# Optimization experiments

Measured on AMD Instinct MI355X. Metric: run time of the kernel, lower is better.

## Reference

```python
import jax, jax.numpy as jnp
import numpy as np

EPS = 1e-6
H = 16
CHUNK = 128

def _fmap(x):
    # elu(x) + 1 positive feature map
    return jax.nn.elu(x) + 1.0

def _causal_lin_attn(Qf, Kf, V, eps):
    # Math-identical chunkwise form of the cumsum causal linear attention.
    B, Hh, N, D = Qf.shape
    Dv = V.shape[-1]
    nc = N // CHUNK
    qs = jnp.moveaxis(Qf.reshape(B, Hh, nc, CHUNK, D), 2, 0)
    ks = jnp.moveaxis(Kf.reshape(B, Hh, nc, CHUNK, D), 2, 0)
    vs = jnp.moveaxis(V.reshape(B, Hh, nc, CHUNK, Dv), 2, 0)
    mask = jnp.tril(jnp.ones((CHUNK, CHUNK), dtype=bool))  # inclusive causal within chunk
    S0 = jnp.zeros((B, Hh, D, Dv), Qf.dtype)
    z0 = jnp.zeros((B, Hh, D), Qf.dtype)

    def step(carry, xs):
        S, z = carry
        q, k, v = xs  # (B,H,C,D), (B,H,C,D), (B,H,C,Dv)
        A = jnp.einsum('bhqd,bhkd->bhqk', q, k)
        A = jnp.where(mask, A, 0.0)
        num = jnp.einsum('bhqd,bhdv->bhqv', q, S) + jnp.einsum('bhqk,bhkv->bhqv', A, v)
        den = jnp.einsum('bhqd,bhd->bhq', q, z) + A.sum(-1)
        out = num / (den[..., None] + eps)
        S = S + jnp.einsum('bhkd,bhkv->bhdv', k, v)
        z = z + k.sum(2)
        return (S, z), out

    _, out = jax.lax.scan(step, (S0, z0), (qs, ks, vs))
    return jnp.moveaxis(out, 0, 2).reshape(B, Hh, N, Dv)

def _mhla(Q, K, V, Wq, Wk, Wv, Wo, causal):
    B, N, E = Q.shape
    D = E // H
    q = (Q @ Wq.T).reshape(B, N, H, D).transpose(0, 2, 1, 3)  # (B,H,N,D)
    k = (K @ Wk.T).reshape(B, N, H, D).transpose(0, 2, 1, 3)
    v = (V @ Wv.T).reshape(B, N, H, D).transpose(0, 2, 1, 3)
    Qf, Kf = _fmap(q), _fmap(k)
    if causal:
        out = _causal_lin_attn(Qf, Kf, v, EPS)
    else:
        KV = jnp.einsum('bhnd,bhnv->bhdv', Kf, v)
        ksum = Kf.sum(2)
        num = jnp.einsum('bhnd,bhdv->bhnv', Qf, KV)
        den = jnp.einsum('bhnd,bhd->bhn', Qf, ksum)[..., None]
        out = num / (den + EPS)
    out = out.transpose(0, 2, 1, 3).reshape(B, N, E)
    return out @ Wo.T

def setup_inputs():
    key = jax.random.key(0)
    ks = jax.random.split(key, 7)
    B, N, E = 2, 2048, 1024

    def xavier(k, shape):
        lim = (6.0 / (shape[0] + shape[1])) ** 0.5
        return jax.random.uniform(k, shape, jnp.float32, -lim, lim)

    return {
        'Q': jax.random.normal(ks[0], (B, N, E), jnp.float32),
        'K': jax.random.normal(ks[1], (B, N, E), jnp.float32),
        'V': jax.random.normal(ks[2], (B, N, E), jnp.float32),
        'Wq': xavier(ks[3], (E, E)),
        'Wk': xavier(ks[4], (E, E)),
        'Wv': xavier(ks[5], (E, E)),
        'Wo': xavier(ks[6], (E, E)),
        'causal': 1,
    }

def reference(Q, K, V, Wq, Wk, Wv, Wo, causal):
    return _mhla(Q, K, V, Wq, Wk, Wv, Wo, causal)
```

## Files before the change

kernel.cpp:

```cpp
#include <hip/hip_runtime.h>
#include <hip/hip_bf16.h>
#include <stdint.h>

#define B_   2
#define N_   2048
#define E_   1024
#define H_   16
#define D_   64
#define CH_  128
#define NC_  16
#define BH_  32
#define M_   4096
#define K_   1024
#define EPS_F 1e-6f

typedef __attribute__((ext_vector_type(8))) __bf16 bf16x8;
typedef __attribute__((ext_vector_type(4))) float  f32x4;

static __device__ __forceinline__ f32x4 mfma16(bf16x8 a, bf16x8 b, f32x4 c) {
  return __builtin_amdgcn_mfma_f32_16x16x32_bf16(a, b, c, 0, 0, 0);
}

static __device__ __forceinline__ unsigned short f2bf(float f) {
  union { float fv; unsigned int u; } x; x.fv = f;
  unsigned int r = x.u + 0x7FFFu + ((x.u >> 16) & 1u);
  return (unsigned short)(r >> 16);
}
static __device__ __forceinline__ float fmap(float x) {
  return x > 0.f ? (x + 1.f) : __expf(x);
}
static __device__ __forceinline__ void gload16(const void* g, void* l) {
  __builtin_amdgcn_global_load_lds(
      (const __attribute__((address_space(1))) void*)g,
      (__attribute__((address_space(3))) void*)l, 16, 0, 0);
}

__global__ __launch_bounds__(256)
void conv_kernel(const float* __restrict__ Q, const float* __restrict__ Kx,
                 const float* __restrict__ V, const float* __restrict__ Wq,
                 const float* __restrict__ Wk, const float* __restrict__ Wv,
                 const float* __restrict__ Wo,
                 unsigned short* __restrict__ Xb, unsigned short* __restrict__ Wb) {
  int gid = blockIdx.x * 256 + threadIdx.x;
  int idx = gid * 4;
  const float* src; unsigned short* dst; int off;
  if (idx < (3 << 22)) {
    int which = idx >> 22;
    off = idx & ((1 << 22) - 1);
    src = (which == 0) ? Q : (which == 1) ? Kx : V;
    dst = Xb + ((size_t)which << 22);
  } else {
    int j = idx - (3 << 22);
    int which = j >> 20;
    off = j & ((1 << 20) - 1);
    src = (which == 0) ? Wq : (which == 1) ? Wk : (which == 2) ? Wv : Wo;
    dst = Wb + ((size_t)which << 20);
  }
  float4 v = *(const float4*)(src + off);
  ushort4 o;
  o.x = f2bf(v.x); o.y = f2bf(v.y); o.z = f2bf(v.z); o.w = f2bf(v.w);
  *(ushort4*)(dst + off) = o;
}

template<int MODE>
__global__ __launch_bounds__(256)
void gemm_kernel(const unsigned short* __restrict__ Aall,
                 const unsigned short* __restrict__ Wall,
                 unsigned short* __restrict__ qf,
                 unsigned short* __restrict__ kf,
                 unsigned short* __restrict__ kt,
                 unsigned short* __restrict__ vt,
                 float* __restrict__ outf) {
  constexpr int BM = (MODE == 0) ? 128 : 64;
  constexpr int WM = BM / 32;
  constexpr int NWG = (MODE == 0) ? 768 : 512;
  __shared__ __align__(16) unsigned short As[BM * 32];
  __shared__ __align__(16) unsigned short Bs[128 * 32];

  const int wg = (blockIdx.x & 7) * (NWG >> 3) + (blockIdx.x >> 3);
  const int nb = wg & 7;
  const int mb = (MODE == 0) ? ((wg >> 3) & 31) : (wg >> 3);
  const int z  = (MODE == 0) ? (wg >> 8) : 3;

  const unsigned short* Ag = Aall + ((MODE == 0) ? ((size_t)z << 22) : 0);
  const unsigned short* Bg = Wall + ((size_t)z << 20);
  const int tid = threadIdx.x;
  const int w = tid >> 6, l = tid & 63;
  const int wm = w >> 1, wn = w & 1;
  const int fl = l & 15, fh = l >> 4;
  const int lrow = l >> 2;
  const int swz = (l & 3) ^ ((l >> 3) & 3);

  const unsigned short* gA = Ag + (size_t)(mb * BM + w * (BM / 4) + lrow) * K_ + swz * 8;
  const unsigned short* gB = Bg + (size_t)(nb * 128 + w * 32 + lrow) * K_ + swz * 8;
  unsigned short* lA = As + w * (BM / 4) * 32;
  unsigned short* lB = Bs + w * 1024;

  const int rs = (fh ^ ((fl >> 1) & 3)) * 8;

  f32x4 acc[WM][4] = {};

  for (int k0 = 0; k0 < K_; k0 += 32) {
    __syncthreads();
    gload16(gA + k0, lA);
    if (MODE == 0) gload16(gA + k0 + 16 * K_, lA + 512);
    gload16(gB + k0, lB);
    gload16(gB + k0 + 16 * K_, lB + 512);
    __syncthreads();
    bf16x8 av[WM], bv[4];
#pragma unroll
    for (int i = 0; i < WM; i++)
      av[i] = *(const bf16x8*)(As + (wm * (BM / 2) + i * 16 + fl) * 32 + rs);
#pragma unroll
    for (int j = 0; j < 4; j++)
      bv[j] = *(const bf16x8*)(Bs + (wn * 64 + j * 16 + fl) * 32 + rs);
#pragma unroll
    for (int i = 0; i < WM; i++)
#pragma unroll
      for (int j = 0; j < 4; j++)
        acc[i][j] = mfma16(av[i], bv[j], acc[i][j]);
  }

#pragma unroll
  for (int i = 0; i < WM; i++)
#pragma unroll
    for (int j = 0; j < 4; j++)
#pragma unroll
      for (int r = 0; r < 4; r++) {
        int m = mb * BM + wm * (BM / 2) + i * 16 + fh * 4 + r;
        int e = nb * 128 + wn * 64 + j * 16 + fl;
        float v = acc[i][j][r];
        if (MODE == 1) {
          outf[(size_t)m * E_ + e] = v;
        } else {
          int b = m >> 11, n = m & (N_ - 1), h = e >> 6, d = e & 63;
          int bh = b * H_ + h;
          if (z == 0) {
            qf[((size_t)bh * N_ + n) * D_ + d] = f2bf(fmap(v));
          } else if (z == 1) {
            unsigned short s = f2bf(fmap(v));
            kf[((size_t)bh * N_ + n) * D_ + d] = s;
            kt[((size_t)bh * D_ + d) * N_ + n] = s;
          } else {
            vt[((size_t)bh * D_ + d) * N_ + n] = f2bf(v);
          }
        }
      }
}

__global__ __launch_bounds__(64)
void chunkkv_kernel(const unsigned short* __restrict__ kt,
                    const unsigned short* __restrict__ vt,
                    float* __restrict__ Sc, float* __restrict__ zc) {
  const int bh = blockIdx.x, c = blockIdx.y;
  const int l = threadIdx.x;
  const int fl = l & 15, fh = l >> 4;
  const int n0 = c * CH_;
  const unsigned short* ktb = kt + (size_t)bh * D_ * N_;
  const unsigned short* vtb = vt + (size_t)bh * D_ * N_;
  f32x4 acc[4][4] = {};
#pragma unroll
  for (int ks = 0; ks < 4; ks++) {
    bf16x8 av[4], bv[4];
#pragma unroll
    for (int i = 0; i < 4; i++)
      av[i] = *(const bf16x8*)(vtb + (size_t)(i * 16 + fl) * N_ + n0 + ks * 32 + fh * 8);
#pragma unroll
    for (int j = 0; j < 4; j++)
      bv[j] = *(const bf16x8*)(ktb + (size_t)(j * 16 + fl) * N_ + n0 + ks * 32 + fh * 8);
#pragma unroll
    for (int i = 0; i < 4; i++)
#pragma unroll
      for (int j = 0; j < 4; j++)
        acc[i][j] = mfma16(av[i], bv[j], acc[i][j]);
  }
  float* Scb = Sc + ((size_t)(bh * NC_ + c) << 12);
#pragma unroll
  for (int i = 0; i < 4; i++)
#pragma unroll
    for (int j = 0; j < 4; j++)
#pragma unroll
      for (int r = 0; r < 4; r++)
        Scb[(i * 16 + fh * 4 + r) * 64 + j * 16 + fl] = acc[i][j][r];
  float s = 0.f;
  const unsigned short* kr = ktb + (size_t)l * N_ + n0;
#pragma unroll
  for (int t = 0; t < 16; t++) {
    bf16x8 v8 = *(const bf16x8*)(kr + t * 8);
#pragma unroll
    for (int e = 0; e < 8; e++) s += (float)v8[e];
  }
  zc[(bh * NC_ + c) * 64 + l] = s;
}

__global__ __launch_bounds__(256)
void prefix_kernel(const float* __restrict__ Sc, const float* __restrict__ zc,
                   unsigned short* __restrict__ St, float* __restrict__ zx) {
  int gid = blockIdx.x * 256 + threadIdx.x;
  if (blockIdx.x < 512) {
    int bh = gid >> 12;
    int idx = gid & 4095;
    float s = 0.f;
    for (int c = 0; c < NC_; c++) {
      size_t base = ((size_t)(bh * NC_ + c)) << 12;
      St[base + idx] = f2bf(s);
      s += Sc[base + idx];
    }
  } else {
    int j = gid - 512 * 256;
    int bh = j >> 6, d = j & 63;
    float s = 0.f;
    for (int c = 0; c < NC_; c++) {
      zx[(bh * NC_ + c) * 64 + d] = s;
      s += zc[(bh * NC_ + c) * 64 + d];
    }
  }
}

__global__ __launch_bounds__(256)
void attn_kernel(const unsigned short* __restrict__ qf,
                 const unsigned short* __restrict__ kf,
                 const unsigned short* __restrict__ vt,
                 const unsigned short* __restrict__ St,
                 const float* __restrict__ zx,
                 unsigned short* __restrict__ AO) {
  __shared__ __align__(16) unsigned short A_lds[128 * 136];
  __shared__ float den_s[128];
  const int c = blockIdx.x, bh = blockIdx.y;
  const int tid = threadIdx.x, w = tid >> 6, l = tid & 63;
  const int fl = l & 15, fh = l >> 4;
  const int n0 = c * CH_;
  const unsigned short* qfb = qf + ((size_t)bh * N_ + n0) * D_;
  const unsigned short* kfb = kf + ((size_t)bh * N_ + n0) * D_;
  const unsigned short* vtb = vt + (size_t)bh * D_ * N_;
  const unsigned short* Stb = St + (((size_t)(bh * NC_ + c)) << 12);
  const float* zxb = zx + (bh * NC_ + c) * 64;

  f32x4 accA[2][8] = {};
#pragma unroll
  for (int ks = 0; ks < 2; ks++) {
    bf16x8 av[2], bv[8];
#pragma unroll
    for (int i = 0; i < 2; i++)
      av[i] = *(const bf16x8*)(qfb + (size_t)(w * 32 + i * 16 + fl) * D_ + ks * 32 + fh * 8);
#pragma unroll
    for (int j = 0; j < 8; j++)
      bv[j] = *(const bf16x8*)(kfb + (size_t)(j * 16 + fl) * D_ + ks * 32 + fh * 8);
#pragma unroll
    for (int i = 0; i < 2; i++)
#pragma unroll
      for (int j = 0; j < 8; j++)
        accA[i][j] = mfma16(av[i], bv[j], accA[i][j]);
  }
#pragma unroll
  for (int i = 0; i < 2; i++)
#pragma unroll
    for (int j = 0; j < 8; j++)
#pragma unroll
      for (int r = 0; r < 4; r++) {
        int qrow = w * 32 + i * 16 + fh * 4 + r;
        int kcol = j * 16 + fl;
        float v = (kcol <= qrow) ? accA[i][j][r] : 0.f;
        A_lds[qrow * 136 + kcol] = f2bf(v);
      }
  __syncthreads();

  if (tid < 128) {
    int row = tid;
    float dq = 0.f;
    const unsigned short* qr = qfb + (size_t)row * D_;
#pragma unroll
    for (int t = 0; t < 8; t++) {
      bf16x8 q8 = *(const bf16x8*)(qr + t * 8);
#pragma unroll
      for (int e = 0; e < 8; e++) dq += (float)q8[e] * zxb[t * 8 + e];
    }
    float ds = 0.f;
#pragma unroll
    for (int t = 0; t < 16; t++) {
      bf16x8 a8 = *(const bf16x8*)(A_lds + row * 136 + t * 8);
#pragma unroll
      for (int e = 0; e < 8; e++) ds += (float)a8[e];
    }
    den_s[row] = dq + ds + EPS_F;
  }
  __syncthreads();

  f32x4 accO[2][4] = {};
#pragma unroll
  for (int ks = 0; ks < 2; ks++) {
    bf16x8 av[2], bv[4];
#pragma unroll
    for (int i = 0; i < 2; i++)
      av[i] = *(const bf16x8*)(qfb + (size_t)(w * 32 + i * 16 + fl) * D_ + ks * 32 + fh * 8);
#pragma unroll
    for (int j = 0; j < 4; j++)
      bv[j] = *(const bf16x8*)(Stb + (j * 16 + fl) * 64 + ks * 32 + fh * 8);
#pragma unroll
    for (int i = 0; i < 2; i++)
#pragma unroll
      for (int j = 0; j < 4; j++)
        accO[i][j] = mfma16(av[i], bv[j], accO[i][j]);
  }
#pragma unroll
  for (int ks = 0; ks < 4; ks++) {
    bf16x8 av[2], bv[4];
#pragma unroll
    for (int i = 0; i < 2; i++)
      av[i] = *(const bf16x8*)(A_lds + (w * 32 + i * 16 + fl) * 136 + ks * 32 + fh * 8);
#pragma unroll
    for (int j = 0; j < 4; j++)
      bv[j] = *(const bf16x8*)(vtb + (size_t)(j * 16 + fl) * N_ + n0 + ks * 32 + fh * 8);
#pragma unroll
    for (int i = 0; i < 2; i++)
#pragma unroll
      for (int j = 0; j < 4; j++)
        accO[i][j] = mfma16(av[i], bv[j], accO[i][j]);
  }

  const int b = bh >> 4, h = bh & 15;
#pragma unroll
  for (int i = 0; i < 2; i++)
#pragma unroll
    for (int j = 0; j < 4; j++)
#pragma unroll
      for (int r = 0; r < 4; r++) {
        int qrow = w * 32 + i * 16 + fh * 4 + r;
        int dv = j * 16 + fl;
        float o = accO[i][j][r] / den_s[qrow];
        AO[((size_t)(b * N_ + n0 + qrow)) * E_ + h * 64 + dv] = f2bf(o);
      }
}

extern "C" void kernel_launch(void* const* d_in, const int* in_sizes, int n_in,
                              void* d_out, int out_size, void* d_ws, size_t ws_size,
                              hipStream_t stream) {
  const float* Q  = (const float*)d_in[0];
  const float* Kx = (const float*)d_in[1];
  const float* V  = (const float*)d_in[2];
  const float* Wq = (const float*)d_in[3];
  const float* Wk = (const float*)d_in[4];
  const float* Wv = (const float*)d_in[5];
  const float* Wo = (const float*)d_in[6];

  char* p = (char*)d_ws;
  unsigned short* Xb = (unsigned short*)p; p += (size_t)3 * M_ * K_ * 2;
  unsigned short* Wb = (unsigned short*)p; p += (size_t)4 * E_ * E_ * 2;
  unsigned short* qf = (unsigned short*)p; p += (size_t)BH_ * N_ * D_ * 2;
  unsigned short* kf = (unsigned short*)p; p += (size_t)BH_ * N_ * D_ * 2;
  unsigned short* kt = (unsigned short*)p; p += (size_t)BH_ * N_ * D_ * 2;
  unsigned short* vt = (unsigned short*)p; p += (size_t)BH_ * N_ * D_ * 2;
  float*          Sc = (float*)p;          p += (size_t)BH_ * NC_ * D_ * D_ * 4;
  float*          zc = (float*)p;          p += (size_t)BH_ * NC_ * D_ * 4;
  unsigned short* St = (unsigned short*)p; p += (size_t)BH_ * NC_ * D_ * D_ * 2;
  float*          zx = (float*)p;          p += (size_t)BH_ * NC_ * D_ * 4;
  unsigned short* AO = (unsigned short*)p; p += (size_t)M_ * E_ * 2;

  conv_kernel<<<dim3(16384), dim3(256), 0, stream>>>(Q, Kx, V, Wq, Wk, Wv, Wo, Xb, Wb);
  gemm_kernel<0><<<dim3(768), dim3(256), 0, stream>>>(Xb, Wb, qf, kf, kt, vt, nullptr);
  chunkkv_kernel<<<dim3(32, 16), dim3(64), 0, stream>>>(kt, vt, Sc, zc);
  prefix_kernel<<<dim3(520), dim3(256), 0, stream>>>(Sc, zc, St, zx);
  attn_kernel<<<dim3(16, 32), dim3(256), 0, stream>>>(qf, kf, vt, St, zx, AO);
  gemm_kernel<1><<<dim3(512), dim3(256), 0, stream>>>(AO, Wb, nullptr, nullptr,
                                                      nullptr, nullptr, (float*)d_out);
}
```

Measured before the change: 214.4 us.

## Fuse chunk-state prefix sum into attention kernel and widen GEMM K-tile

The separate prefix_kernel is removed. Each attention block now sums the preceding chunks' KV states and key sums directly from Sc/zc into LDS, stored as swizzled bf16, which removes one launch and the St/zx round trip through global memory. The cost is redundant reads that grow with chunk index. The GEMM K-step is doubled to 64 with a new XOR swizzle and two MFMA substeps per load, halving the barrier count per K. The denominator reduction is also split across all 256 threads instead of 128.

```diff
diff --git a/kernel.cpp b/kernel.cpp
--- a/kernel.cpp
+++ b/kernel.cpp
@@ -73,9 +73,10 @@
                  float* __restrict__ outf) {
   constexpr int BM = (MODE == 0) ? 128 : 64;
   constexpr int WM = BM / 32;
+  constexpr int RA = BM / 32;
   constexpr int NWG = (MODE == 0) ? 768 : 512;
-  __shared__ __align__(16) unsigned short As[BM * 32];
-  __shared__ __align__(16) unsigned short Bs[128 * 32];
+  __shared__ __align__(16) unsigned short As[BM * 64];
+  __shared__ __align__(16) unsigned short Bs[128 * 64];
 
   const int wg = (blockIdx.x & 7) * (NWG >> 3) + (blockIdx.x >> 3);
   const int nb = wg & 7;
@@ -88,37 +89,42 @@
   const int w = tid >> 6, l = tid & 63;
   const int wm = w >> 1, wn = w & 1;
   const int fl = l & 15, fh = l >> 4;
-  const int lrow = l >> 2;
-  const int swz = (l & 3) ^ ((l >> 3) & 3);
-
-  const unsigned short* gA = Ag + (size_t)(mb * BM + w * (BM / 4) + lrow) * K_ + swz * 8;
-  const unsigned short* gB = Bg + (size_t)(nb * 128 + w * 32 + lrow) * K_ + swz * 8;
-  unsigned short* lA = As + w * (BM / 4) * 32;
-  unsigned short* lB = Bs + w * 1024;
-
-  const int rs = (fh ^ ((fl >> 1) & 3)) * 8;
+
+  const int srow  = w * 8 + (l >> 3);
+  const int sslot = (l & 7) ^ (l >> 3);
+  const unsigned short* gA = Ag + (size_t)(mb * BM + srow) * K_ + sslot * 8;
+  const unsigned short* gB = Bg + (size_t)(nb * 128 + srow) * K_ + sslot * 8;
+
+  const int rswz = (fl & 7) << 3;
 
   f32x4 acc[WM][4] = {};
 
-  for (int k0 = 0; k0 < K_; k0 += 32) {
+  for (int k0 = 0; k0 < K_; k0 += 64) {
     __syncthreads();
-    gload16(gA + k0, lA);
-    if (MODE == 0) gload16(gA + k0 + 16 * K_, lA + 512);
-    gload16(gB + k0, lB);
-    gload16(gB + k0 + 16 * K_, lB + 512);
+#pragma unroll
+    for (int r = 0; r < RA; r++)
+      gload16(gA + (size_t)r * 32 * K_ + k0, As + (r * 32 + w * 8) * 64);
+#pragma unroll
+    for (int r = 0; r < 4; r++)
+      gload16(gB + (size_t)r * 32 * K_ + k0, Bs + (r * 32 + w * 8) * 64);
     __syncthreads();
-    bf16x8 av[WM], bv[4];
-#pragma unroll
-    for (int i = 0; i < WM; i++)
-      av[i] = *(const bf16x8*)(As + (wm * (BM / 2) + i * 16 + fl) * 32 + rs);
-#pragma unroll
-    for (int j = 0; j < 4; j++)
-      bv[j] = *(const bf16x8*)(Bs + (wn * 64 + j * 16 + fl) * 32 + rs);
-#pragma unroll
-    for (int i = 0; i < WM; i++)
+#pragma unroll
+    for (int kk = 0; kk < 2; kk++) {
+      bf16x8 av[WM], bv[4];
+#pragma unroll
+      for (int i = 0; i < WM; i++)
+        av[i] = *(const bf16x8*)(As + (wm * (BM / 2) + i * 16 + fl) * 64
+                                    + ((kk * 32 + fh * 8) ^ rswz));
 #pragma unroll
       for (int j = 0; j < 4; j++)
-        acc[i][j] = mfma16(av[i], bv[j], acc[i][j]);
+        bv[j] = *(const bf16x8*)(Bs + (wn * 64 + j * 16 + fl) * 64
+                                    + ((kk * 32 + fh * 8) ^ rswz));
+#pragma unroll
+      for (int i = 0; i < WM; i++)
+#pragma unroll
+        for (int j = 0; j < 4; j++)
+          acc[i][j] = mfma16(av[i], bv[j], acc[i][j]);
+    }
   }
 
 #pragma unroll
@@ -194,38 +200,16 @@
 }
 
 __global__ __launch_bounds__(256)
-void prefix_kernel(const float* __restrict__ Sc, const float* __restrict__ zc,
-                   unsigned short* __restrict__ St, float* __restrict__ zx) {
-  int gid = blockIdx.x * 256 + threadIdx.x;
-  if (blockIdx.x < 512) {
-    int bh = gid >> 12;
-    int idx = gid & 4095;
-    float s = 0.f;
-    for (int c = 0; c < NC_; c++) {
-      size_t base = ((size_t)(bh * NC_ + c)) << 12;
-      St[base + idx] = f2bf(s);
-      s += Sc[base + idx];
-    }
-  } else {
-    int j = gid - 512 * 256;
-    int bh = j >> 6, d = j & 63;
-    float s = 0.f;
-    for (int c = 0; c < NC_; c++) {
-      zx[(bh * NC_ + c) * 64 + d] = s;
-      s += zc[(bh * NC_ + c) * 64 + d];
-    }
-  }
-}
-
-__global__ __launch_bounds__(256)
 void attn_kernel(const unsigned short* __restrict__ qf,
                  const unsigned short* __restrict__ kf,
                  const unsigned short* __restrict__ vt,
-                 const unsigned short* __restrict__ St,
-                 const float* __restrict__ zx,
+                 const float* __restrict__ Sc,
+                 const float* __restrict__ zc,
                  unsigned short* __restrict__ AO) {
   __shared__ __align__(16) unsigned short A_lds[128 * 136];
-  __shared__ float den_s[128];
+  __shared__ __align__(16) unsigned short St_lds[64 * 64];
+  __shared__ float zx_lds[64];
+  __shared__ float den_s[128][2];
   const int c = blockIdx.x, bh = blockIdx.y;
   const int tid = threadIdx.x, w = tid >> 6, l = tid & 63;
   const int fl = l & 15, fh = l >> 4;
@@ -233,8 +217,6 @@
   const unsigned short* qfb = qf + ((size_t)bh * N_ + n0) * D_;
   const unsigned short* kfb = kf + ((size_t)bh * N_ + n0) * D_;
   const unsigned short* vtb = vt + (size_t)bh * D_ * N_;
-  const unsigned short* Stb = St + (((size_t)(bh * NC_ + c)) << 12);
-  const float* zxb = zx + (bh * NC_ + c) * 64;
 
   f32x4 accA[2][8] = {};
 #pragma unroll
@@ -263,29 +245,51 @@
         float v = (kcol <= qrow) ? accA[i][j][r] : 0.f;
         A_lds[qrow * 136 + kcol] = f2bf(v);
       }
+
+  {
+    float s[16];
+#pragma unroll
+    for (int j = 0; j < 16; j++) s[j] = 0.f;
+    for (int c2 = 0; c2 < c; c2++) {
+      const float* b = Sc + (((size_t)(bh * NC_ + c2)) << 12);
+#pragma unroll
+      for (int j = 0; j < 16; j++) s[j] += b[tid + j * 256];
+    }
+#pragma unroll
+    for (int j = 0; j < 16; j++) {
+      int fi = tid + j * 256;
+      int rw = (fi >> 6) & 7;
+      St_lds[fi ^ (rw << 3)] = f2bf(s[j]);
+    }
+    if (tid < 64) {
+      float zs = 0.f;
+      for (int c2 = 0; c2 < c; c2++) zs += zc[(bh * NC_ + c2) * 64 + tid];
+      zx_lds[tid] = zs;
+    }
+  }
   __syncthreads();
 
-  if (tid < 128) {
-    int row = tid;
+  {
+    int row = tid >> 1, h2 = tid & 1;
     float dq = 0.f;
     const unsigned short* qr = qfb + (size_t)row * D_;
 #pragma unroll
+    for (int t = 0; t < 4; t++) {
+      bf16x8 q8 = *(const bf16x8*)(qr + (h2 * 4 + t) * 8);
+#pragma unroll
+      for (int e = 0; e < 8; e++) dq += (float)q8[e] * zx_lds[(h2 * 4 + t) * 8 + e];
+    }
+#pragma unroll
     for (int t = 0; t < 8; t++) {
-      bf16x8 q8 = *(const bf16x8*)(qr + t * 8);
-#pragma unroll
-      for (int e = 0; e < 8; e++) dq += (float)q8[e] * zxb[t * 8 + e];
-    }
-    float ds = 0.f;
-#pragma unroll
-    for (int t = 0; t < 16; t++) {
-      bf16x8 a8 = *(const bf16x8*)(A_lds + row * 136 + t * 8);
-#pragma unroll
-      for (int e = 0; e < 8; e++) ds += (float)a8[e];
-    }
-    den_s[row] = dq + ds + EPS_F;
+      bf16x8 a8 = *(const bf16x8*)(A_lds + row * 136 + (h2 * 8 + t) * 8);
+#pragma unroll
+      for (int e = 0; e < 8; e++) dq += (float)a8[e];
+    }
+    den_s[row][h2] = dq;
   }
   __syncthreads();
 
+  const int rswz = (fl & 7) << 3;
   f32x4 accO[2][4] = {};
 #pragma unroll
   for (int ks = 0; ks < 2; ks++) {
@@ -295,7 +299,7 @@
       av[i] = *(const bf16x8*)(qfb + (size_t)(w * 32 + i * 16 + fl) * D_ + ks * 32 + fh * 8);
 #pragma unroll
     for (int j = 0; j < 4; j++)
-      bv[j] = *(const bf16x8*)(Stb + (j * 16 + fl) * 64 + ks * 32 + fh * 8);
+      bv[j] = *(const bf16x8*)(St_lds + (j * 16 + fl) * 64 + ((ks * 32 + fh * 8) ^ rswz));
 #pragma unroll
     for (int i = 0; i < 2; i++)
 #pragma unroll
@@ -327,7 +331,8 @@
       for (int r = 0; r < 4; r++) {
         int qrow = w * 32 + i * 16 + fh * 4 + r;
         int dv = j * 16 + fl;
-        float o = accO[i][j][r] / den_s[qrow];
+        float den = den_s[qrow][0] + den_s[qrow][1] + EPS_F;
+        float o = accO[i][j][r] / den;
         AO[((size_t)(b * N_ + n0 + qrow)) * E_ + h * 64 + dv] = f2bf(o);
       }
 }
@@ -352,15 +357,12 @@
   unsigned short* vt = (unsigned short*)p; p += (size_t)BH_ * N_ * D_ * 2;
   float*          Sc = (float*)p;          p += (size_t)BH_ * NC_ * D_ * D_ * 4;
   float*          zc = (float*)p;          p += (size_t)BH_ * NC_ * D_ * 4;
-  unsigned short* St = (unsigned short*)p; p += (size_t)BH_ * NC_ * D_ * D_ * 2;
-  float*          zx = (float*)p;          p += (size_t)BH_ * NC_ * D_ * 4;
   unsigned short* AO = (unsigned short*)p; p += (size_t)M_ * E_ * 2;
 
   conv_kernel<<<dim3(16384), dim3(256), 0, stream>>>(Q, Kx, V, Wq, Wk, Wv, Wo, Xb, Wb);
   gemm_kernel<0><<<dim3(768), dim3(256), 0, stream>>>(Xb, Wb, qf, kf, kt, vt, nullptr);
   chunkkv_kernel<<<dim3(32, 16), dim3(64), 0, stream>>>(kt, vt, Sc, zc);
-  prefix_kernel<<<dim3(520), dim3(256), 0, stream>>>(Sc, zc, St, zx);
-  attn_kernel<<<dim3(16, 32), dim3(256), 0, stream>>>(qf, kf, vt, St, zx, AO);
+  attn_kernel<<<dim3(16, 32), dim3(256), 0, stream>>>(qf, kf, vt, Sc, zc, AO);
   gemm_kernel<1><<<dim3(512), dim3(256), 0, stream>>>(AO, Wb, nullptr, nullptr,
                                                       nullptr, nullptr, (float*)d_out);
 }
```

New measurement: 218.3 us. About the same (+1.8%).
